# Kernel optimization log

Hardware: AMD Instinct MI355X
Metric: run time of the kernel (lower is better)

The kernel has to match this reference:

```python
import math
import jax, jax.numpy as jnp
import numpy as np

FACTOR = 5


def setup_inputs() -> dict:
    key = jax.random.key(0)
    kq, kk, kv, ki = jax.random.split(key, 4)
    B, H, L, D = 4, 8, 2048, 64
    sample_k = min(FACTOR * math.ceil(math.log(L)), L)  # 40
    queries = jax.random.normal(kq, (B, H, L, D), dtype=jnp.float32)
    keys = jax.random.normal(kk, (B, H, L, D), dtype=jnp.float32)
    values = jax.random.normal(kv, (B, H, L, D), dtype=jnp.float32)
    index_sample = jax.random.randint(ki, (L, sample_k), 0, L, dtype=jnp.int64 if jax.config.jax_enable_x64 else jnp.int32)
    return {"queries": queries, "keys": keys, "values": values, "index_sample": index_sample}


def reference(queries, keys, values, index_sample):
    B, H, L_Q, D = queries.shape
    L_K = keys.shape[2]
    u = min(FACTOR * math.ceil(math.log(L_Q)), L_Q)  # n_top queries (= 40)
    scale = 1.0 / math.sqrt(D)

    # --- _prob_QK: sparsity measurement over randomly sampled keys ---
    # K_sample[b,h,q,s,:] = keys[b,h,index_sample[q,s],:]  -> [B,H,L_Q,S,D]
    K_sample = keys[:, :, index_sample, :]
    Q_K_sample = jnp.einsum('bhqd,bhqsd->bhqs', queries, K_sample)  # [B,H,L_Q,S]
    M = Q_K_sample.max(axis=-1) - Q_K_sample.sum(axis=-1) / L_K      # [B,H,L_Q]
    _, M_top = jax.lax.top_k(M, u)                                    # [B,H,u]

    Q_reduce = jnp.take_along_axis(queries, M_top[..., None], axis=2)  # [B,H,u,D]
    scores_top = jnp.einsum('bhud,bhkd->bhuk', Q_reduce, keys) * scale  # [B,H,u,L_K]

    # --- initial context: causal cumulative sum of V (mask_flag=True) ---
    context = jnp.cumsum(values, axis=2)  # [B,H,L_Q,D]

    # --- ProbMask: causal rows gathered at the selected query indices ---
    causal = jnp.triu(jnp.ones((L_Q, L_K), dtype=bool), 1)  # [L_Q,L_K]
    mask = causal[M_top]                                     # [B,H,u,L_K]
    scores_top = jnp.where(mask, -jnp.inf, scores_top)

    attn = jax.nn.softmax(scores_top, axis=-1)                       # [B,H,u,L_K]
    update = jnp.einsum('bhuk,bhkd->bhud', attn, values)             # [B,H,u,D]

    b_idx = jnp.arange(B)[:, None, None]
    h_idx = jnp.arange(H)[None, :, None]
    context = context.at[b_idx, h_idx, M_top].set(update.astype(context.dtype))
    return context
```

## Files before the change

### kernel.cpp

```cpp
#include <hip/hip_runtime.h>
#include <math.h>

#define BB 4
#define HH 8
#define LL 2048
#define DD 64
#define SK 40
#define BH (BB*HH)
#define NC 16
#define CK 128

__device__ __forceinline__ unsigned ordu(float v) {
    unsigned u = __float_as_uint(v);
    return (u & 0x80000000u) ? ~u : (u | 0x80000000u);
}

__device__ __forceinline__ float dot4(float4 a, float4 b) {
    return a.x * b.x + a.y * b.y + a.z * b.z + a.w * b.w;
}

__global__ __launch_bounds__(256) void stage1_kernel(
        const float* __restrict__ Q, const float* __restrict__ K,
        const float* __restrict__ V, const int* __restrict__ IDX,
        float* __restrict__ M, float* __restrict__ csum) {
    int tid = threadIdx.x;
    int b = blockIdx.x;
    int bhLo = b & 7;
    int bhA = bhLo + 8 * ((b >> 3) & 1);
    int bhB = bhA + 16;
    int chunk = b >> 4;
    int qbase = chunk * 64;
    int w = tid >> 6, lane = tid & 63;
    int qw = lane >> 2, c = lane & 3;
    int qi = w * 16 + qw;
    int qpos = qbase + qi;

    __shared__ int sidx[64 * SK];
    __shared__ float part[4][DD];

    for (int i = tid; i < 64 * SK; i += 256) sidx[i] = IDX[(size_t)qbase * SK + i];

    const float4* Q4 = (const float4*)Q;
    const float4* K4 = (const float4*)K;
    float4 qA[4], qB[4];
    #pragma unroll
    for (int j = 0; j < 4; ++j) {
        qA[j] = Q4[((size_t)bhA * LL + qpos) * 16 + j * 4 + c];
        qB[j] = Q4[((size_t)bhB * LL + qpos) * 16 + j * 4 + c];
    }
    __syncthreads();

    size_t kbA = (size_t)bhA * LL * 16;
    size_t kbB = (size_t)bhB * LL * 16;
    float mxA = -INFINITY, smA = 0.f, mxB = -INFINITY, smB = 0.f;

    float4 a0[4], b0[4], a1[4], b1[4];
    {
        int ks = sidx[qi * SK];
        const float4* krA = K4 + kbA + (size_t)ks * 16;
        const float4* krB = K4 + kbB + (size_t)ks * 16;
        #pragma unroll
        for (int j = 0; j < 4; ++j) { a0[j] = krA[j * 4 + c]; b0[j] = krB[j * 4 + c]; }
    }
    for (int s = 0; s < SK; s += 2) {
        {
            int ks = sidx[qi * SK + s + 1];
            const float4* krA = K4 + kbA + (size_t)ks * 16;
            const float4* krB = K4 + kbB + (size_t)ks * 16;
            #pragma unroll
            for (int j = 0; j < 4; ++j) { a1[j] = krA[j * 4 + c]; b1[j] = krB[j * 4 + c]; }
        }
        {
            float pA = dot4(qA[0], a0[0]) + dot4(qA[1], a0[1])
                     + dot4(qA[2], a0[2]) + dot4(qA[3], a0[3]);
            float pB = dot4(qB[0], b0[0]) + dot4(qB[1], b0[1])
                     + dot4(qB[2], b0[2]) + dot4(qB[3], b0[3]);
            pA += __shfl_xor(pA, 1, 64); pA += __shfl_xor(pA, 2, 64);
            pB += __shfl_xor(pB, 1, 64); pB += __shfl_xor(pB, 2, 64);
            mxA = fmaxf(mxA, pA); smA += pA;
            mxB = fmaxf(mxB, pB); smB += pB;
        }
        if (s + 2 < SK) {
            int ks = sidx[qi * SK + s + 2];
            const float4* krA = K4 + kbA + (size_t)ks * 16;
            const float4* krB = K4 + kbB + (size_t)ks * 16;
            #pragma unroll
            for (int j = 0; j < 4; ++j) { a0[j] = krA[j * 4 + c]; b0[j] = krB[j * 4 + c]; }
        }
        {
            float pA = dot4(qA[0], a1[0]) + dot4(qA[1], a1[1])
                     + dot4(qA[2], a1[2]) + dot4(qA[3], a1[3]);
            float pB = dot4(qB[0], b1[0]) + dot4(qB[1], b1[1])
                     + dot4(qB[2], b1[2]) + dot4(qB[3], b1[3]);
            pA += __shfl_xor(pA, 1, 64); pA += __shfl_xor(pA, 2, 64);
            pB += __shfl_xor(pB, 1, 64); pB += __shfl_xor(pB, 2, 64);
            mxA = fmaxf(mxA, pA); smA += pA;
            mxB = fmaxf(mxB, pB); smB += pB;
        }
    }
    if (c == 0) {
        M[(size_t)bhA * LL + qpos] = mxA - smA * (1.0f / (float)LL);
        M[(size_t)bhB * LL + qpos] = mxB - smB * (1.0f / (float)LL);
    }

    {
        int bhv = (b & 7) + 8 * ((b >> 3) & 3);
        int cv = b >> 5;
        int d = tid & 63, sg = tid >> 6;
        size_t base = (size_t)bhv * LL * DD;
        int row0 = cv * 128 + sg * 32;
        float s2 = 0.f;
        for (int j = 0; j < 32; ++j) s2 += V[base + (size_t)(row0 + j) * DD + d];
        part[sg][d] = s2;
        __syncthreads();
        if (sg == 0)
            csum[((size_t)bhv * 16 + cv) * DD + d] =
                part[0][d] + part[1][d] + part[2][d] + part[3][d];
    }
}

__global__ __launch_bounds__(256) void attn_cumsum_kernel(
        const float* __restrict__ Q, const float* __restrict__ K,
        const float* __restrict__ V, const float* __restrict__ M,
        const float* __restrict__ csum, float* __restrict__ out,
        float* __restrict__ pm, float* __restrict__ pl,
        float* __restrict__ po, int* __restrict__ topk) {
    int tid = threadIdx.x;
    __shared__ int qp[SK];
    __shared__ float4 sq4[SK][16];
    __shared__ float SC[CK][SK + 1];
    __shared__ float part[4][DD];
    __shared__ unsigned hist[256], sfx[256];
    __shared__ int eqlist[128], qtmp[SK];
    __shared__ unsigned bc_prefix, bc_need, cnt_gt, cnt_eq;

    if (blockIdx.x < 512) {
        int x = blockIdx.x;
        int bhLo = x & 7;
        int r = x >> 3;
        int c = r & 15;
        int bhHi = r >> 4;
        int bh = bhHi * 8 + bhLo;
        int w = tid >> 6, lane = tid & 63;
        int cbase = c * CK;

        unsigned v[8];
        #pragma unroll
        for (int j = 0; j < 8; ++j)
            v[j] = ordu(M[(size_t)bh * LL + tid + j * 256]);

        unsigned prefix = 0, need = SK;
        #pragma unroll
        for (int pass = 0; pass < 4; ++pass) {
            const int s = 24 - 8 * pass;
            const unsigned maskHigh = (pass == 0) ? 0u : (0xFFFFFFFFu << (s + 8));
            hist[tid] = 0;
            __syncthreads();
            #pragma unroll
            for (int j = 0; j < 8; ++j)
                if (((v[j] ^ prefix) & maskHigh) == 0)
                    atomicAdd(&hist[(v[j] >> s) & 0xFF], 1u);
            __syncthreads();
            sfx[tid] = hist[tid];
            __syncthreads();
            #pragma unroll
            for (int off = 1; off < 256; off <<= 1) {
                unsigned t = (tid + off < 256) ? sfx[tid + off] : 0u;
                __syncthreads();
                sfx[tid] += t;
                __syncthreads();
            }
            unsigned above = (tid < 255) ? sfx[tid + 1] : 0u;
            if (above < need && sfx[tid] >= need) {
                bc_prefix = prefix | ((unsigned)tid << s);
                bc_need = need - above;
            }
            __syncthreads();
            prefix = bc_prefix;
            need = bc_need;
            __syncthreads();
        }
        unsigned T = prefix;
        if (tid == 0) { cnt_gt = 0; cnt_eq = 0; }
        __syncthreads();
        #pragma unroll
        for (int j = 0; j < 8; ++j) {
            int idx = tid + j * 256;
            if (v[j] > T) { unsigned p = atomicAdd(&cnt_gt, 1u); qtmp[p] = idx; }
            else if (v[j] == T) { unsigned p = atomicAdd(&cnt_eq, 1u); if (p < 128) eqlist[p] = idx; }
        }
        __syncthreads();
        if (tid == 0) {
            int ne = (int)min(cnt_eq, 128u);
            unsigned base = cnt_gt;
            for (unsigned r2 = 0; r2 < need; ++r2) {
                int bj = 0, bv = 0x7FFFFFFF;
                for (int j = 0; j < ne; ++j)
                    if (eqlist[j] < bv) { bv = eqlist[j]; bj = j; }
                qtmp[base + r2] = bv;
                eqlist[bj] = 0x7FFFFFFF;
            }
        }
        __syncthreads();
        if (tid < SK) {
            int mine = qtmp[tid];
            int rank = 0;
            for (int j = 0; j < SK; ++j) rank += (qtmp[j] < mine);
            qp[rank] = mine;
        }
        __syncthreads();
        if (c == 0 && tid < SK) topk[bh * SK + tid] = qp[tid];

        const float4* Q4 = (const float4*)Q;
        const float4* K4 = (const float4*)K;
        const float4* V4 = (const float4*)V;
        for (int i = tid; i < SK * 16; i += 256) {
            int u = i >> 4, j = i & 15;
            sq4[u][j] = Q4[((size_t)bh * LL + qp[u]) * 16 + j];
        }
        __syncthreads();

        {
            int half = tid & 1;
            int kk = tid >> 1;
            int kg = cbase + kk;
            size_t kb4 = (size_t)bh * LL * 16;
            float4 kreg[8];
            const float4* kr = K4 + kb4 + (size_t)kg * 16 + half * 8;
            #pragma unroll
            for (int j = 0; j < 8; ++j) kreg[j] = kr[j];
            #pragma unroll 4
            for (int u = 0; u < SK; ++u) {
                int qpu = qp[u];
                if (cbase > qpu) {
                    if (half == 0) SC[kk][u] = -INFINITY;
                    continue;
                }
                float pa = 0.f, pb = 0.f;
                #pragma unroll
                for (int j = 0; j < 4; ++j) {
                    float4 qv = sq4[u][half * 8 + j];
                    pa += kreg[j].x * qv.x + kreg[j].y * qv.y + kreg[j].z * qv.z + kreg[j].w * qv.w;
                }
                #pragma unroll
                for (int j = 4; j < 8; ++j) {
                    float4 qv = sq4[u][half * 8 + j];
                    pb += kreg[j].x * qv.x + kreg[j].y * qv.y + kreg[j].z * qv.z + kreg[j].w * qv.w;
                }
                float p = pa + pb;
                p += __shfl_xor(p, 1, 64);
                if (half == 0) SC[kk][u] = (kg <= qpu) ? p * 0.125f : -INFINITY;
            }
        }
        __syncthreads();

        for (int u = w; u < SK; u += 4) {
            float s0 = SC[lane][u], s1 = SC[lane + 64][u];
            float m = fmaxf(s0, s1);
            #pragma unroll
            for (int off = 32; off > 0; off >>= 1) m = fmaxf(m, __shfl_xor(m, off, 64));
            float e0 = 0.f, e1 = 0.f;
            if (m != -INFINITY) {
                e0 = expf(s0 - m);
                e1 = expf(s1 - m);
            }
            SC[lane][u] = e0;
            SC[lane + 64][u] = e1;
            float ls = e0 + e1;
            #pragma unroll
            for (int off = 32; off > 0; off >>= 1) ls += __shfl_xor(ls, off, 64);
            if (lane == 0) {
                size_t pb = (size_t)(bh * SK + u) * NC + c;
                pm[pb] = m;
                pl[pb] = ls;
            }
        }
        __syncthreads();

        {
            int ks = tid & 3;
            int dg = (tid >> 2) & 15;
            int ug = tid >> 6;
            int u0 = ug * 10;
            float4 acc[10];
            #pragma unroll
            for (int i = 0; i < 10; ++i) acc[i] = make_float4(0.f, 0.f, 0.f, 0.f);
            for (int t = 0; t < CK / 4; ++t) {
                int k = t * 4 + ks;
                float4 vv = V4[((size_t)bh * LL + cbase + k) * 16 + dg];
                #pragma unroll
                for (int i = 0; i < 10; ++i) {
                    float pw = SC[k][u0 + i];
                    acc[i].x += pw * vv.x; acc[i].y += pw * vv.y;
                    acc[i].z += pw * vv.z; acc[i].w += pw * vv.w;
                }
            }
            #pragma unroll
            for (int i = 0; i < 10; ++i) {
                acc[i].x += __shfl_xor(acc[i].x, 1, 64); acc[i].x += __shfl_xor(acc[i].x, 2, 64);
                acc[i].y += __shfl_xor(acc[i].y, 1, 64); acc[i].y += __shfl_xor(acc[i].y, 2, 64);
                acc[i].z += __shfl_xor(acc[i].z, 1, 64); acc[i].z += __shfl_xor(acc[i].z, 2, 64);
                acc[i].w += __shfl_xor(acc[i].w, 1, 64); acc[i].w += __shfl_xor(acc[i].w, 2, 64);
            }
            if (ks == 0) {
                #pragma unroll
                for (int i = 0; i < 10; ++i) {
                    float4* dst = (float4*)&po[((size_t)(bh * SK + u0 + i) * NC + c) * DD + dg * 4];
                    *dst = acc[i];
                }
            }
        }
    } else {
        int x = blockIdx.x - 512;
        int bhLo = x & 7, r = x >> 3;
        int bhHi = r & 3, c = r >> 2;
        int bh = bhHi * 8 + bhLo;
        int d = tid & 63, sg = tid >> 6;
        size_t base = (size_t)bh * LL * DD;
        int row0 = c * 128 + sg * 32;
        float v[32];
        #pragma unroll
        for (int j = 0; j < 32; ++j) v[j] = V[base + (size_t)(row0 + j) * DD + d];
        float s = 0.f;
        #pragma unroll
        for (int j = 0; j < 32; ++j) s += v[j];
        part[sg][d] = s;
        __syncthreads();
        float pre = 0.f;
        for (int cc = 0; cc < c; ++cc) pre += csum[((size_t)bh * 16 + cc) * DD + d];
        for (int ss = 0; ss < sg; ++ss) pre += part[ss][d];
        float acc = pre;
        #pragma unroll
        for (int j = 0; j < 32; ++j) {
            acc += v[j];
            out[base + (size_t)(row0 + j) * DD + d] = acc;
        }
    }
}

__global__ __launch_bounds__(256) void combine_kernel(
        const float* __restrict__ pm, const float* __restrict__ pl,
        const float* __restrict__ po, const int* __restrict__ topk,
        float* __restrict__ out) {
    int g = blockIdx.x * 4 + (threadIdx.x >> 6);
    int d = threadIdx.x & 63;
    int qpos = topk[g];
    int bh = g / SK;
    size_t gb = (size_t)g * NC;
    float gm = -INFINITY;
    #pragma unroll
    for (int j = 0; j < NC; ++j) gm = fmaxf(gm, pm[gb + j]);
    float L = 0.f, o = 0.f;
    #pragma unroll
    for (int j = 0; j < NC; ++j) {
        float pmj = pm[gb + j];
        float wj = (pmj == -INFINITY) ? 0.f : expf(pmj - gm);
        L += pl[gb + j] * wj;
        o += po[(gb + j) * DD + d] * wj;
    }
    out[((size_t)bh * LL + qpos) * DD + d] = o / L;
}

extern "C" void kernel_launch(void* const* d_in, const int* in_sizes, int n_in,
                              void* d_out, int out_size, void* d_ws, size_t ws_size,
                              hipStream_t stream) {
    const float* Q   = (const float*)d_in[0];
    const float* K   = (const float*)d_in[1];
    const float* V   = (const float*)d_in[2];
    const int*   IDX = (const int*)d_in[3];
    float* out = (float*)d_out;

    char* ws = (char*)d_ws;
    float* M    = (float*)ws;  ws += (size_t)BH * LL * sizeof(float);
    int*   topk = (int*)ws;    ws += ((size_t)BH * SK * sizeof(int) + 255) & ~255ull;
    float* csum = (float*)ws;  ws += (size_t)BH * 16 * DD * sizeof(float);
    float* pm   = (float*)ws;  ws += ((size_t)BH * SK * NC * sizeof(float) + 255) & ~255ull;
    float* pl   = (float*)ws;  ws += ((size_t)BH * SK * NC * sizeof(float) + 255) & ~255ull;
    float* po   = (float*)ws;

    stage1_kernel<<<512, 256, 0, stream>>>(Q, K, V, IDX, M, csum);
    attn_cumsum_kernel<<<1024, 256, 0, stream>>>(Q, K, V, M, csum, out, pm, pl, po, topk);
    combine_kernel<<<320, 256, 0, stream>>>(pm, pl, po, topk, out);
}
```

Before: 157.9 us.

## Move top-k radix select into its own kernel instead of per-block recompute

Previously every one of the 512 attention blocks redid the full radix top-k selection for its batch-head, so each selection was repeated 16 times. A new 32-block radix_kernel now computes the top-k query indices once per batch-head and writes them to global memory. The attention kernel just loads them, which frees its histogram and scratch shared memory. The cost is an extra launch and a small, low-occupancy serial stage. The rank-sort step is also dropped, so the indices are no longer in ascending order, which matters if later code assumes sorted positions.

```diff
diff --git a/kernel.cpp b/kernel.cpp
--- a/kernel.cpp
+++ b/kernel.cpp
@@ -119,20 +119,86 @@
     }
 }
 
+__global__ __launch_bounds__(256) void radix_kernel(
+        const float* __restrict__ M, int* __restrict__ topk) {
+    int tid = threadIdx.x;
+    int bh = blockIdx.x;
+    __shared__ unsigned hist[256];
+    __shared__ unsigned sfx[256];
+    __shared__ unsigned bc_prefix, bc_need;
+    __shared__ unsigned cnt_gt, cnt_eq;
+    __shared__ int eqlist[128];
+
+    unsigned v[8];
+    #pragma unroll
+    for (int j = 0; j < 8; ++j)
+        v[j] = ordu(M[(size_t)bh * LL + tid + j * 256]);
+
+    unsigned prefix = 0, need = SK;
+    #pragma unroll
+    for (int pass = 0; pass < 4; ++pass) {
+        const int s = 24 - 8 * pass;
+        const unsigned maskHigh = (pass == 0) ? 0u : (0xFFFFFFFFu << (s + 8));
+        hist[tid] = 0;
+        __syncthreads();
+        #pragma unroll
+        for (int j = 0; j < 8; ++j)
+            if (((v[j] ^ prefix) & maskHigh) == 0)
+                atomicAdd(&hist[(v[j] >> s) & 0xFF], 1u);
+        __syncthreads();
+        sfx[tid] = hist[tid];
+        __syncthreads();
+        #pragma unroll
+        for (int off = 1; off < 256; off <<= 1) {
+            unsigned t = (tid + off < 256) ? sfx[tid + off] : 0u;
+            __syncthreads();
+            sfx[tid] += t;
+            __syncthreads();
+        }
+        unsigned above = (tid < 255) ? sfx[tid + 1] : 0u;
+        if (above < need && sfx[tid] >= need) {
+            bc_prefix = prefix | ((unsigned)tid << s);
+            bc_need = need - above;
+        }
+        __syncthreads();
+        prefix = bc_prefix;
+        need = bc_need;
+        __syncthreads();
+    }
+    unsigned T = prefix;
+    if (tid == 0) { cnt_gt = 0; cnt_eq = 0; }
+    __syncthreads();
+    #pragma unroll
+    for (int j = 0; j < 8; ++j) {
+        int idx = tid + j * 256;
+        if (v[j] > T) { unsigned p = atomicAdd(&cnt_gt, 1u); topk[bh * SK + p] = idx; }
+        else if (v[j] == T) { unsigned p = atomicAdd(&cnt_eq, 1u); if (p < 128) eqlist[p] = idx; }
+    }
+    __syncthreads();
+    if (tid == 0) {
+        int ne = (int)min(cnt_eq, 128u);
+        unsigned base = cnt_gt;
+        for (unsigned r2 = 0; r2 < need; ++r2) {
+            int bj = 0, bv = 0x7FFFFFFF;
+            for (int j = 0; j < ne; ++j)
+                if (eqlist[j] < bv) { bv = eqlist[j]; bj = j; }
+            topk[bh * SK + base + r2] = bv;
+            eqlist[bj] = 0x7FFFFFFF;
+        }
+    }
+}
+
 __global__ __launch_bounds__(256) void attn_cumsum_kernel(
         const float* __restrict__ Q, const float* __restrict__ K,
-        const float* __restrict__ V, const float* __restrict__ M,
+        const float* __restrict__ V, const int* __restrict__ topk,
         const float* __restrict__ csum, float* __restrict__ out,
         float* __restrict__ pm, float* __restrict__ pl,
-        float* __restrict__ po, int* __restrict__ topk) {
+        float* __restrict__ po) {
     int tid = threadIdx.x;
     __shared__ int qp[SK];
     __shared__ float4 sq4[SK][16];
     __shared__ float SC[CK][SK + 1];
     __shared__ float part[4][DD];
-    __shared__ unsigned hist[256], sfx[256];
-    __shared__ int eqlist[128], qtmp[SK];
-    __shared__ unsigned bc_prefix, bc_need, cnt_gt, cnt_eq;
 
     if (blockIdx.x < 512) {
         int x = blockIdx.x;
@@ -144,73 +210,8 @@
         int w = tid >> 6, lane = tid & 63;
         int cbase = c * CK;
 
-        unsigned v[8];
-        #pragma unroll
-        for (int j = 0; j < 8; ++j)
-            v[j] = ordu(M[(size_t)bh * LL + tid + j * 256]);
-
-        unsigned prefix = 0, need = SK;
-        #pragma unroll
-        for (int pass = 0; pass < 4; ++pass) {
-            const int s = 24 - 8 * pass;
-            const unsigned maskHigh = (pass == 0) ? 0u : (0xFFFFFFFFu << (s + 8));
-            hist[tid] = 0;
-            __syncthreads();
-            #pragma unroll
-            for (int j = 0; j < 8; ++j)
-                if (((v[j] ^ prefix) & maskHigh) == 0)
-                    atomicAdd(&hist[(v[j] >> s) & 0xFF], 1u);
-            __syncthreads();
-            sfx[tid] = hist[tid];
-            __syncthreads();
-            #pragma unroll
-            for (int off = 1; off < 256; off <<= 1) {
-                unsigned t = (tid + off < 256) ? sfx[tid + off] : 0u;
-                __syncthreads();
-                sfx[tid] += t;
-                __syncthreads();
-            }
-            unsigned above = (tid < 255) ? sfx[tid + 1] : 0u;
-            if (above < need && sfx[tid] >= need) {
-                bc_prefix = prefix | ((unsigned)tid << s);
-                bc_need = need - above;
-            }
-            __syncthreads();
-            prefix = bc_prefix;
-            need = bc_need;
-            __syncthreads();
-        }
-        unsigned T = prefix;
-        if (tid == 0) { cnt_gt = 0; cnt_eq = 0; }
-        __syncthreads();
-        #pragma unroll
-        for (int j = 0; j < 8; ++j) {
-            int idx = tid + j * 256;
-            if (v[j] > T) { unsigned p = atomicAdd(&cnt_gt, 1u); qtmp[p] = idx; }
-            else if (v[j] == T) { unsigned p = atomicAdd(&cnt_eq, 1u); if (p < 128) eqlist[p] = idx; }
-        }
-        __syncthreads();
-        if (tid == 0) {
-            int ne = (int)min(cnt_eq, 128u);
-            unsigned base = cnt_gt;
-            for (unsigned r2 = 0; r2 < need; ++r2) {
-                int bj = 0, bv = 0x7FFFFFFF;
-                for (int j = 0; j < ne; ++j)
-                    if (eqlist[j] < bv) { bv = eqlist[j]; bj = j; }
-                qtmp[base + r2] = bv;
-                eqlist[bj] = 0x7FFFFFFF;
-            }
-        }
-        __syncthreads();
-        if (tid < SK) {
-            int mine = qtmp[tid];
-            int rank = 0;
-            for (int j = 0; j < SK; ++j) rank += (qtmp[j] < mine);
-            qp[rank] = mine;
-        }
-        __syncthreads();
-        if (c == 0 && tid < SK) topk[bh * SK + tid] = qp[tid];
-
+        if (tid < SK) qp[tid] = topk[bh * SK + tid];
+        __syncthreads();
         const float4* Q4 = (const float4*)Q;
         const float4* K4 = (const float4*)K;
         const float4* V4 = (const float4*)V;
@@ -379,6 +380,7 @@
     float* po   = (float*)ws;
 
     stage1_kernel<<<512, 256, 0, stream>>>(Q, K, V, IDX, M, csum);
-    attn_cumsum_kernel<<<1024, 256, 0, stream>>>(Q, K, V, M, csum, out, pm, pl, po, topk);
+    radix_kernel<<<32, 256, 0, stream>>>(M, topk);
+    attn_cumsum_kernel<<<1024, 256, 0, stream>>>(Q, K, V, topk, csum, out, pm, pl, po);
     combine_kernel<<<320, 256, 0, stream>>>(pm, pl, po, topk, out);
 }
```

Result: faster. 154.1 us (-2.4%).
